# Performance work log

Measured on AMD Instinct MI355X. Metric: run time of the kernel, lower is better.

## Reference

```python
import jax, jax.numpy as jnp
import numpy as np

K = 64        # num_clusters
S1 = 5        # num_shadow + 1
C = 128       # dim
ALPHA = 1500.0
EPS = 1e-12


def setup_inputs() -> dict:
    key = jax.random.key(0)
    k1, k2 = jax.random.split(key)
    x = jax.random.normal(k1, (8, C, 44, 44), dtype=jnp.float32)
    centroids = jax.random.normal(k2, (K, S1, C), dtype=jnp.float32) * 0.01
    return {"x": x, "centroids": centroids}


def reference(x, centroids):
    N = x.shape[0]
    # conv params derived from centroids, as in _init_params
    w = (2.0 * ALPHA) * centroids.reshape(K * S1, C)            # (K*S1, C)
    b = -ALPHA * jnp.linalg.norm(centroids.reshape(K * S1, C), axis=1)  # (K*S1,)

    xf = x.reshape(N, C, -1)                                    # (N, C, P)
    # 1x1 conv == GEMM over channel dim
    logits = jnp.einsum('mc,ncp->nmp', w, xf) + b[None, :, None]
    logits = logits.reshape(N, K, S1, -1)                       # (N, K, S1, P)

    soft_alpha = jax.nn.softmax(logits[:, :, 0:1, :], axis=1)   # (N, K, 1, P)
    soft_beta = jax.nn.softmax(logits, axis=2)[:, :, 0:1, :]    # (N, K, 1, P)
    soft_assign = soft_alpha * soft_beta                        # (N, K, 1, P)

    # residual = x - rep_centroid; then residual *= (1 + soft_assign); sum over P.
    # sum_p (x[n,c,p] - rep[k,c]) * w[n,k,p]
    #   = einsum(w, x) - rep[k,c] * sum_p w[n,k,p]   (same math, no (N,K,C,P) tensor)
    w_assign = 1.0 + soft_assign[:, :, 0, :]                    # (N, K, P)
    rep = centroids[:, 0, :]                                    # (K, C)
    out = jnp.einsum('nkp,ncp->nkc', w_assign, xf) \
          - rep[None, :, :] * jnp.sum(w_assign, axis=-1)[:, :, None]  # (N, K, C)

    # intra-cluster L2 normalize (dim=2), flatten, global L2 normalize
    out = out / jnp.maximum(jnp.linalg.norm(out, axis=2, keepdims=True), EPS)
    flat = out.reshape(N, -1)
    flat = flat / jnp.maximum(jnp.linalg.norm(flat, axis=1, keepdims=True), EPS)
    return (flat, soft_assign)
```

## Files before the change

### kernel.cpp

```cpp
#include <hip/hip_runtime.h>
#include <math.h>

#define NB 8
#define KC 64
#define S1C 5
#define CC 128
#define PP 1936
#define MM 320
#define PT 64
#define NPT 31
#define NTILE (NB * NPT)
#define ALPHAF 1500.0f
#define EPSF 1e-12f

#define WS_CENPK 65536
#define WS_GBIAS 512
#define WS_HDR   (WS_CENPK + WS_GBIAS)
#define WS_PART  ((size_t)NTILE * KC * CC)
#define WS_MAIN_FLOATS (WS_HDR + WS_PART + (size_t)NTILE * KC)

typedef __attribute__((ext_vector_type(8))) short short8;
typedef __attribute__((ext_vector_type(4))) float f32x4;

__device__ __forceinline__ void split8(const float4 a, const float4 b,
                                       short8& h, short8& l) {
    const float f[8] = {a.x, a.y, a.z, a.w, b.x, b.y, b.z, b.w};
#pragma unroll
    for (int j = 0; j < 8; ++j) {
        const unsigned u  = __float_as_uint(f[j]);
        const unsigned hi = u & 0xffff0000u;
        const float lo    = f[j] - __uint_as_float(hi);
        h[j] = (short)(hi >> 16);
        l[j] = (short)(__float_as_uint(lo) >> 16);
    }
}

__global__ __launch_bounds__(64) void k0_pack(
    const float* __restrict__ cen, unsigned* __restrict__ cenPk,
    float* __restrict__ gbias)
{
    const int nt   = blockIdx.x;
    const int l    = threadIdx.x;
    const int l15  = l & 15;
    const int quad = l >> 4;
    const int mp   = nt * 16 + l15;
    const int s    = mp & 7;
    const bool valid = (s < 5);
    const int wrow = 5 * (mp >> 3) + s;
    short8* dst8 = (short8*)cenPk;
    float ss = 0.f;
#pragma unroll
    for (int ks = 0; ks < 4; ++ks) {
        float4 v0 = make_float4(0.f, 0.f, 0.f, 0.f), v1 = v0;
        if (valid) {
            const float* wp = cen + (size_t)wrow * CC + ks * 32 + quad * 8;
            v0 = *(const float4*)wp;
            v1 = *(const float4*)(wp + 4);
        }
        ss += v0.x * v0.x + v0.y * v0.y + v0.z * v0.z + v0.w * v0.w
            + v1.x * v1.x + v1.y * v1.y + v1.z * v1.z + v1.w * v1.w;
        short8 h, lo;
        split8(v0, v1, h, lo);
        const int base = ((ks * 32 + nt) * 64 + l) * 2;
        dst8[base]     = h;
        dst8[base + 1] = lo;
    }
    ss += __shfl_xor(ss, 16);
    ss += __shfl_xor(ss, 32);
    if (quad == 0) gbias[mp] = valid ? (-ALPHAF * sqrtf(ss)) : -3.0e38f;
}

__global__ __launch_bounds__(1024, 4) void k1_main(
    const float* __restrict__ x, const unsigned* __restrict__ cenPk,
    const float* __restrict__ gbias,
    float* __restrict__ sa_out, float* __restrict__ outC,
    float* __restrict__ outS, int mode)
{
    __shared__ __align__(16) unsigned short xh [64 * 128];
    __shared__ __align__(16) unsigned short xl [64 * 128];
    __shared__ __align__(16) unsigned short xch[128 * 64];
    __shared__ __align__(16) unsigned short xcl[128 * 64];
    __shared__ __align__(16) unsigned short wah[64 * 64];
    __shared__ __align__(16) unsigned short wal[64 * 64];
    __shared__ float2 ap[16 * 66];

    const int tid  = threadIdx.x;
    const int lane = tid & 63;
    const int wid  = tid >> 6;
    const int quad = lane >> 4;
    const int l15  = lane & 15;
    const int bx   = blockIdx.x;
    const int n    = bx / NPT;
    const int pt   = bx - n * NPT;
    const int p0   = pt * PT;

    float4 bvf[2];
#pragma unroll
    for (int i = 0; i < 2; ++i)
        bvf[i] = *(const float4*)(gbias + (2 * wid + i) * 16 + quad * 4);
    const short8* cpk8 = (const short8*)cenPk;
    short8 ch0[2], cl0[2];
#pragma unroll
    for (int i = 0; i < 2; ++i) {
        const int boff = ((2 * wid + i) * 64 + lane) * 2;
        ch0[i] = cpk8[boff];
        cl0[i] = cpk8[boff + 1];
    }

    const float* xn = x + (size_t)n * CC * PP;
    {
        const int pl = tid & 63;
        const int c0 = (tid >> 6) * 8;
        const bool pv = (p0 + pl) < PP;
        const float* src = xn + p0 + pl;
        float v[8];
#pragma unroll
        for (int i = 0; i < 8; ++i)
            v[i] = pv ? src[(size_t)(c0 + i) * PP] : 0.f;
        unsigned short hv[8], lv[8];
#pragma unroll
        for (int i = 0; i < 8; ++i) {
            const unsigned u  = __float_as_uint(v[i]);
            const unsigned hi = u & 0xffff0000u;
            hv[i] = (unsigned short)(hi >> 16);
            lv[i] = (unsigned short)(__float_as_uint(v[i] - __uint_as_float(hi)) >> 16);
        }
        short8 H8, L8;
#pragma unroll
        for (int i = 0; i < 8; ++i) { H8[i] = (short)hv[i]; L8[i] = (short)lv[i]; }
        const int sx = (pl * 128 + c0) ^ ((pl & 7) << 3);
        *(short8*)&xh[sx] = H8;
        *(short8*)&xl[sx] = L8;
#pragma unroll
        for (int i = 0; i < 8; ++i) {
            const int ci  = c0 + i;
            const int sc2 = (ci * 64 + pl) ^ ((ci & 7) << 3);
            xch[sc2] = hv[i];
            xcl[sc2] = lv[i];
        }
    }
    __syncthreads();

    f32x4 dacc[4][2];
#pragma unroll
    for (int a = 0; a < 4; ++a) {
        dacc[a][0] = (f32x4){0.f, 0.f, 0.f, 0.f};
        dacc[a][1] = (f32x4){0.f, 0.f, 0.f, 0.f};
    }

    auto mfma_step = [&](const int ksoff, const short8 ch[2], const short8 cl[2]) {
#pragma unroll
        for (int a = 0; a < 4; ++a) {
            const int arow = a * 16 + l15;
            const int sidx = (arow * 128 + ksoff + quad * 8) ^ ((arow & 7) << 3);
            const short8 xh8 = *(const short8*)&xh[sidx];
            const short8 xl8 = *(const short8*)&xl[sidx];
#pragma unroll
            for (int i = 0; i < 2; ++i) {
                dacc[a][i] = __builtin_amdgcn_mfma_f32_16x16x32_bf16(ch[i], xh8, dacc[a][i], 0, 0, 0);
                dacc[a][i] = __builtin_amdgcn_mfma_f32_16x16x32_bf16(ch[i], xl8, dacc[a][i], 0, 0, 0);
                dacc[a][i] = __builtin_amdgcn_mfma_f32_16x16x32_bf16(cl[i], xh8, dacc[a][i], 0, 0, 0);
            }
        }
    };

    mfma_step(0, ch0, cl0);
#pragma unroll 1
    for (int ks = 1; ks < 4; ++ks) {
        short8 ch[2], cl[2];
#pragma unroll
        for (int i = 0; i < 2; ++i) {
            const int boff = ((ks * 32 + 2 * wid + i) * 64 + lane) * 2;
            ch[i] = cpk8[boff];
            cl[i] = cpk8[boff + 1];
        }
        mfma_step(ks * 32, ch, cl);
    }

#pragma unroll
    for (int i = 0; i < 2; ++i) {
        const float* bvp = (const float*)&bvf[i];
#pragma unroll
        for (int a = 0; a < 4; ++a)
#pragma unroll
            for (int r = 0; r < 4; ++r)
                dacc[a][i][r] = 2.f * ALPHAF * dacc[a][i][r] + bvp[r];
    }

#pragma unroll
    for (int a = 0; a < 4; ++a) {
        const float l0 = dacc[a][0][0];
        const float l1 = dacc[a][1][0];
        const float m2 = fmaxf(l0, l1);
        const float mo = __shfl_xor(m2, 32);
        const float m4 = fmaxf(m2, mo);
        float se = __expf(l0 - m4) + __expf(l1 - m4);
        se += __shfl_xor(se, 32);
        if ((lane & 48) == 0) ap[wid * 66 + a * 16 + l15] = make_float2(m4, se);
    }
    __syncthreads();

    float gmv, arv;
    {
        float gm = -3.0e38f;
#pragma unroll
        for (int w = 0; w < 16; ++w) gm = fmaxf(gm, ap[w * 66 + lane].x);
        float s = 0.f;
#pragma unroll
        for (int w = 0; w < 16; ++w) {
            const float2 v = ap[w * 66 + lane];
            s += v.y * __expf(v.x - gm);
        }
        gmv = gm; arv = 1.0f / s;
    }

    const int  kb  = 4 * wid + ((lane >> 5) & 1);
    const bool evq = ((lane & 16) == 0);
    float psum2[2] = {0.f, 0.f};
#pragma unroll
    for (int a = 0; a < 4; ++a) {
        const int p = a * 16 + l15;
        const float gm_p = __shfl(gmv, p);
        const float ar_p = __shfl(arv, p);
        const bool pvalid = (p0 + p) < PP;
#pragma unroll
        for (int i = 0; i < 2; ++i) {
            const f32x4 lg = dacc[a][i];
            const float s4 = __shfl_xor(lg[0], 16);
            float m5 = fmaxf(fmaxf(lg[0], lg[1]), fmaxf(lg[2], lg[3]));
            m5 = fmaxf(m5, s4);
            const float e0 = __expf(lg[0] - m5);
            const float d5 = e0 + __expf(lg[1] - m5) + __expf(lg[2] - m5)
                           + __expf(lg[3] - m5) + __expf(s4 - m5);
            const float sa = __expf(lg[0] - gm_p) * ar_p * (e0 / d5);
            const float wa = pvalid ? (1.0f + sa) : 0.0f;
            if (evq) {
                const int kk = kb + 2 * i;
                const int si = (kk * 64 + p) ^ ((kk & 7) << 3);
                const unsigned u  = __float_as_uint(wa);
                const unsigned hi = u & 0xffff0000u;
                wah[si] = (unsigned short)(hi >> 16);
                wal[si] = (unsigned short)(__float_as_uint(wa - __uint_as_float(hi)) >> 16);
            }
            psum2[i] += wa;
        }
    }
#pragma unroll
    for (int i = 0; i < 2; ++i) {
        float s = psum2[i];
        s += __shfl_xor(s, 1);
        s += __shfl_xor(s, 2);
        s += __shfl_xor(s, 4);
        s += __shfl_xor(s, 8);
        if ((lane & 31) == 0) {
            const int k = kb + 2 * i;
            if (mode == 0) outS[(size_t)bx * KC + k] = s;
            else           atomicAdd(&outS[(size_t)n * KC + k], s);
        }
    }
    __syncthreads();

    const int kt  = wid & 3;
    const int ct0 = (wid >> 2) * 2;
    f32x4 cacc[2];
    cacc[0] = (f32x4){0.f, 0.f, 0.f, 0.f};
    cacc[1] = (f32x4){0.f, 0.f, 0.f, 0.f};
#pragma unroll
    for (int ks = 0; ks < 64; ks += 32) {
        const int arow = kt * 16 + l15;
        const int sa_  = (arow * 64 + ks + quad * 8) ^ ((arow & 7) << 3);
        const short8 ah = *(const short8*)&wah[sa_];
        const short8 al = *(const short8*)&wal[sa_];
#pragma unroll
        for (int t = 0; t < 2; ++t) {
            const int crow = (ct0 + t) * 16 + l15;
            const int sb   = (crow * 64 + ks + quad * 8) ^ ((crow & 7) << 3);
            const short8 bh = *(const short8*)&xch[sb];
            const short8 bl = *(const short8*)&xcl[sb];
            cacc[t] = __builtin_amdgcn_mfma_f32_16x16x32_bf16(ah, bh, cacc[t], 0, 0, 0);
            cacc[t] = __builtin_amdgcn_mfma_f32_16x16x32_bf16(ah, bl, cacc[t], 0, 0, 0);
            cacc[t] = __builtin_amdgcn_mfma_f32_16x16x32_bf16(al, bh, cacc[t], 0, 0, 0);
        }
    }
    if (mode == 0) {
        float* dst = outC + (size_t)bx * KC * CC;
#pragma unroll
        for (int t = 0; t < 2; ++t) {
            const int c = (ct0 + t) * 16 + l15;
#pragma unroll
            for (int r = 0; r < 4; ++r)
                dst[(kt * 16 + 4 * quad + r) * CC + c] = cacc[t][r];
        }
    } else {
        float* dst = outC + (size_t)n * KC * CC;
#pragma unroll
        for (int t = 0; t < 2; ++t) {
            const int c = (ct0 + t) * 16 + l15;
#pragma unroll
            for (int r = 0; r < 4; ++r)
                atomicAdd(&dst[(kt * 16 + 4 * quad + r) * CC + c], cacc[t][r]);
        }
    }

    {
        float* san = sa_out + (size_t)n * KC * PP;
        const int k  = tid >> 4;
        const int p4 = (tid & 15) * 4;
        const int pg = p0 + p4;
        if (pg < PP) {
            const int si = (k * 64 + p4) ^ ((k & 7) << 3);
            const uint2 qh = *(const uint2*)&wah[si];
            const uint2 ql = *(const uint2*)&wal[si];
            const unsigned hh[2] = {qh.x, qh.y};
            const unsigned ll[2] = {ql.x, ql.y};
            float4 sv; float* svp = &sv.x;
#pragma unroll
            for (int j = 0; j < 4; ++j) {
                const unsigned h16 = (hh[j >> 1] >> ((j & 1) * 16)) & 0xffffu;
                const unsigned l16 = (ll[j >> 1] >> ((j & 1) * 16)) & 0xffffu;
                const float wa = __uint_as_float(h16 << 16) + __uint_as_float(l16 << 16);
                svp[j] = wa - 1.0f;
            }
            *(float4*)&san[(size_t)k * PP + pg] = sv;
        }
    }
}

__global__ __launch_bounds__(128) void k2_slab(
    const float* __restrict__ part, const float* __restrict__ ps,
    const float* __restrict__ cen, float* __restrict__ flat)
{
    __shared__ float w2[2];
    const int b = blockIdx.x;
    const int n = b >> 6;
    const int k = b & 63;
    const int c = threadIdx.x;
    const float* pb = part + (size_t)n * NPT * KC * CC + (size_t)k * CC + c;
    float v = 0.f;
#pragma unroll 8
    for (int pt = 0; pt < NPT; ++pt) v += pb[(size_t)pt * KC * CC];
    const float* psb = ps + (size_t)n * NPT * KC + k;
    float sw = 0.f;
#pragma unroll
    for (int pt = 0; pt < NPT; ++pt) sw += psb[(size_t)pt * KC];
    v -= cen[(size_t)k * S1C * CC + c] * sw;

    float ss = v * v;
#pragma unroll
    for (int off = 32; off > 0; off >>= 1) ss += __shfl_down(ss, off);
    if ((c & 63) == 0) w2[c >> 6] = ss;
    __syncthreads();
    const float norm = sqrtf(w2[0] + w2[1]);
    const float scale = 1.0f / (fmaxf(norm, EPSF) * 8.0f);
    flat[(size_t)b * CC + c] = v * scale;
}

__global__ __launch_bounds__(128) void k2_final(
    const float* __restrict__ accC, const float* __restrict__ accS,
    const float* __restrict__ cen, float* __restrict__ flat)
{
    __shared__ float w2[2];
    const int b = blockIdx.x;
    const int k = b & 63;
    const int c = threadIdx.x;
    const float v = accC[(size_t)b * CC + c] -
                    cen[(size_t)k * S1C * CC + c] * accS[b];
    float ss = v * v;
#pragma unroll
    for (int off = 32; off > 0; off >>= 1) ss += __shfl_down(ss, off);
    if ((c & 63) == 0) w2[c >> 6] = ss;
    __syncthreads();
    const float norm = sqrtf(w2[0] + w2[1]);
    const float scale = 1.0f / (fmaxf(norm, EPSF) * 8.0f);
    flat[(size_t)b * CC + c] = v * scale;
}

extern "C" void kernel_launch(void* const* d_in, const int* in_sizes, int n_in,
                              void* d_out, int out_size, void* d_ws, size_t ws_size,
                              hipStream_t stream) {
    const float* x   = (const float*)d_in[0];
    const float* cen = (const float*)d_in[1];
    float* out  = (float*)d_out;
    float* flat = out;
    float* sa   = out + (size_t)NB * KC * CC;
    float* ws   = (float*)d_ws;

    unsigned* cenPk = (unsigned*)ws;
    float*    gbias = ws + WS_CENPK;

    if (ws_size >= WS_MAIN_FLOATS * 4) {
        float* part = ws + WS_HDR;
        float* ps   = part + WS_PART;
        k0_pack<<<32, 64, 0, stream>>>(cen, cenPk, gbias);
        k1_main<<<NTILE, 1024, 0, stream>>>(x, cenPk, gbias, sa, part, ps, 0);
        k2_slab<<<NB * KC, 128, 0, stream>>>(part, ps, cen, flat);
    } else {
        float* accC = ws + WS_HDR;
        float* accS = accC + (size_t)NB * KC * CC;
        hipMemsetAsync(accC, 0, (size_t)(NB * KC * CC + NB * KC) * 4, stream);
        k0_pack<<<32, 64, 0, stream>>>(cen, cenPk, gbias);
        k1_main<<<NTILE, 1024, 0, stream>>>(x, cenPk, gbias, sa, accC, accS, 1);
        k2_final<<<NB * KC, 128, 0, stream>>>(accC, accS, cen, flat);
    }
}
```

Measured before the change: 81.56 us.

## Fuse pack, main, and slab kernels into one persistent kernel with grid barriers

```diff
diff --git a/kernel.cpp b/kernel.cpp
--- a/kernel.cpp
+++ b/kernel.cpp
@@ -6,7 +6,6 @@
 #define S1C 5
 #define CC 128
 #define PP 1936
-#define MM 320
 #define PT 64
 #define NPT 31
 #define NTILE (NB * NPT)
@@ -17,7 +16,9 @@
 #define WS_GBIAS 512
 #define WS_HDR   (WS_CENPK + WS_GBIAS)
 #define WS_PART  ((size_t)NTILE * KC * CC)
-#define WS_MAIN_FLOATS (WS_HDR + WS_PART + (size_t)NTILE * KC)
+#define WS_BAR   (WS_HDR + WS_PART + (size_t)NTILE * KC)
+#define WS_TOTAL (WS_BAR + 4)
+#define BAR_MAGIC 0x9E3779B97F4A7C15ull
 
 typedef __attribute__((ext_vector_type(8))) short short8;
 typedef __attribute__((ext_vector_type(4))) float f32x4;
@@ -35,12 +36,27 @@
     }
 }
 
-__global__ __launch_bounds__(64) void k0_pack(
+__device__ __forceinline__ void gbar(unsigned* cnt, unsigned* gen, unsigned nblk) {
+    __syncthreads();
+    if (threadIdx.x == 0) {
+        __threadfence();
+        const unsigned g = __hip_atomic_load(gen, __ATOMIC_ACQUIRE, __HIP_MEMORY_SCOPE_AGENT);
+        const unsigned old = __hip_atomic_fetch_add(cnt, 1u, __ATOMIC_ACQ_REL, __HIP_MEMORY_SCOPE_AGENT);
+        if (old == nblk - 1u) {
+            __hip_atomic_store(cnt, 0u, __ATOMIC_RELAXED, __HIP_MEMORY_SCOPE_AGENT);
+            __hip_atomic_fetch_add(gen, 1u, __ATOMIC_RELEASE, __HIP_MEMORY_SCOPE_AGENT);
+        } else {
+            while (__hip_atomic_load(gen, __ATOMIC_ACQUIRE, __HIP_MEMORY_SCOPE_AGENT) == g)
+                __builtin_amdgcn_s_sleep(8);
+        }
+    }
+    __syncthreads();
+}
+
+__device__ __forceinline__ void k0_body(
     const float* __restrict__ cen, unsigned* __restrict__ cenPk,
-    float* __restrict__ gbias)
+    float* __restrict__ gbias, const int nt, const int l)
 {
-    const int nt   = blockIdx.x;
-    const int l    = threadIdx.x;
     const int l15  = l & 15;
     const int quad = l >> 4;
     const int mp   = nt * 16 + l15;
@@ -70,11 +86,17 @@
     if (quad == 0) gbias[mp] = valid ? (-ALPHAF * sqrtf(ss)) : -3.0e38f;
 }
 
-__global__ __launch_bounds__(1024, 4) void k1_main(
-    const float* __restrict__ x, const unsigned* __restrict__ cenPk,
-    const float* __restrict__ gbias,
-    float* __restrict__ sa_out, float* __restrict__ outC,
-    float* __restrict__ outS, int mode)
+__global__ __launch_bounds__(64) void k0_pack(
+    const float* __restrict__ cen, unsigned* __restrict__ cenPk,
+    float* __restrict__ gbias)
+{
+    k0_body(cen, cenPk, gbias, blockIdx.x, threadIdx.x);
+}
+
+__global__ __launch_bounds__(1024, 4) void k_fused(
+    const float* __restrict__ x, const float* __restrict__ cen,
+    float* __restrict__ ws, float* __restrict__ sa_out,
+    float* __restrict__ flat)
 {
     __shared__ __align__(16) unsigned short xh [64 * 128];
     __shared__ __align__(16) unsigned short xl [64 * 128];
@@ -83,6 +105,15 @@
     __shared__ __align__(16) unsigned short wah[64 * 64];
     __shared__ __align__(16) unsigned short wal[64 * 64];
     __shared__ float2 ap[16 * 66];
+    __shared__ float  shw[16];
+
+    unsigned*  cenPk = (unsigned*)ws;
+    float*     gbias = ws + WS_CENPK;
+    float*     part  = ws + WS_HDR;
+    float*     ps    = part + WS_PART;
+    unsigned*  bcnt  = (unsigned*)(ws + WS_BAR);
+    unsigned*  bgen  = bcnt + 1;
+    unsigned long long* bready = (unsigned long long*)(bcnt + 2);
 
     const int tid  = threadIdx.x;
     const int lane = tid & 63;
@@ -94,18 +125,7 @@
     const int pt   = bx - n * NPT;
     const int p0   = pt * PT;
 
-    float4 bvf[2];
-#pragma unroll
-    for (int i = 0; i < 2; ++i)
-        bvf[i] = *(const float4*)(gbias + (2 * wid + i) * 16 + quad * 4);
-    const short8* cpk8 = (const short8*)cenPk;
-    short8 ch0[2], cl0[2];
-#pragma unroll
-    for (int i = 0; i < 2; ++i) {
-        const int boff = ((2 * wid + i) * 64 + lane) * 2;
-        ch0[i] = cpk8[boff];
-        cl0[i] = cpk8[boff + 1];
-    }
+    if (bx < 32 && tid < 64) k0_body(cen, cenPk, gbias, bx, tid);
 
     const float* xn = x + (size_t)n * CC * PP;
     {
@@ -139,7 +159,34 @@
             xcl[sc2] = lv[i];
         }
     }
-    __syncthreads();
+
+    if (tid == 0) {
+        if (bx == 0) {
+            if (__hip_atomic_load(bready, __ATOMIC_ACQUIRE, __HIP_MEMORY_SCOPE_AGENT) != BAR_MAGIC) {
+                __hip_atomic_store(bcnt, 0u, __ATOMIC_RELAXED, __HIP_MEMORY_SCOPE_AGENT);
+                __hip_atomic_store(bgen, 0u, __ATOMIC_RELAXED, __HIP_MEMORY_SCOPE_AGENT);
+                __hip_atomic_store(bready, (unsigned long long)BAR_MAGIC,
+                                   __ATOMIC_RELEASE, __HIP_MEMORY_SCOPE_AGENT);
+            }
+        } else {
+            while (__hip_atomic_load(bready, __ATOMIC_ACQUIRE, __HIP_MEMORY_SCOPE_AGENT) != BAR_MAGIC)
+                __builtin_amdgcn_s_sleep(8);
+        }
+    }
+    gbar(bcnt, bgen, NTILE);
+
+    float4 bvf[2];
+#pragma unroll
+    for (int i = 0; i < 2; ++i)
+        bvf[i] = *(const float4*)(gbias + (2 * wid + i) * 16 + quad * 4);
+    const short8* cpk8 = (const short8*)cenPk;
+    short8 ch0[2], cl0[2];
+#pragma unroll
+    for (int i = 0; i < 2; ++i) {
+        const int boff = ((2 * wid + i) * 64 + lane) * 2;
+        ch0[i] = cpk8[boff];
+        cl0[i] = cpk8[boff + 1];
+    }
 
     f32x4 dacc[4][2];
 #pragma unroll
@@ -252,11 +299,8 @@
         s += __shfl_xor(s, 2);
         s += __shfl_xor(s, 4);
         s += __shfl_xor(s, 8);
-        if ((lane & 31) == 0) {
-            const int k = kb + 2 * i;
-            if (mode == 0) outS[(size_t)bx * KC + k] = s;
-            else           atomicAdd(&outS[(size_t)n * KC + k], s);
-        }
+        if ((lane & 31) == 0)
+            ps[(size_t)bx * KC + kb + 2 * i] = s;
     }
     __syncthreads();
 
@@ -282,23 +326,14 @@
             cacc[t] = __builtin_amdgcn_mfma_f32_16x16x32_bf16(al, bh, cacc[t], 0, 0, 0);
         }
     }
-    if (mode == 0) {
-        float* dst = outC + (size_t)bx * KC * CC;
+    {
+        float* dst = part + (size_t)bx * KC * CC;
 #pragma unroll
         for (int t = 0; t < 2; ++t) {
             const int c = (ct0 + t) * 16 + l15;
 #pragma unroll
             for (int r = 0; r < 4; ++r)
                 dst[(kt * 16 + 4 * quad + r) * CC + c] = cacc[t][r];
-        }
-    } else {
-        float* dst = outC + (size_t)n * KC * CC;
-#pragma unroll
-        for (int t = 0; t < 2; ++t) {
-            const int c = (ct0 + t) * 16 + l15;
-#pragma unroll
-            for (int r = 0; r < 4; ++r)
-                atomicAdd(&dst[(kt * 16 + 4 * quad + r) * CC + c], cacc[t][r]);
         }
     }
 
@@ -324,35 +359,271 @@
             *(float4*)&san[(size_t)k * PP + pg] = sv;
         }
     }
-}
-
-__global__ __launch_bounds__(128) void k2_slab(
-    const float* __restrict__ part, const float* __restrict__ ps,
-    const float* __restrict__ cen, float* __restrict__ flat)
+
+    gbar(bcnt, bgen, NTILE);
+
+    if (bx < 64) {
+        const int slab = bx * 8 + (tid >> 7);
+        const int sn = slab >> 6;
+        const int sk = slab & 63;
+        const int c  = tid & 127;
+        const float* pb = part + (size_t)sn * NPT * KC * CC + (size_t)sk * CC + c;
+        float v = 0.f;
+#pragma unroll 8
+        for (int q = 0; q < NPT; ++q) v += pb[(size_t)q * KC * CC];
+        const float* psb = ps + (size_t)sn * NPT * KC + sk;
+        float sw = 0.f;
+#pragma unroll
+        for (int q = 0; q < NPT; ++q) sw += psb[(size_t)q * KC];
+        v -= cen[(size_t)sk * S1C * CC + c] * sw;
+
+        float ss = v * v;
+#pragma unroll
+        for (int off = 32; off > 0; off >>= 1) ss += __shfl_down(ss, off);
+        if ((c & 63) == 0) shw[(tid >> 7) * 2 + ((c >> 6) & 1)] = ss;
+        __syncthreads();
+        const float norm = sqrtf(shw[(tid >> 7) * 2] + shw[(tid >> 7) * 2 + 1]);
+        const float scale = 1.0f / (fmaxf(norm, EPSF) * 8.0f);
+        flat[(size_t)slab * CC + c] = v * scale;
+    }
+}
+
+__global__ __launch_bounds__(1024, 4) void k1_atomic(
+    const float* __restrict__ x, const unsigned* __restrict__ cenPk,
+    const float* __restrict__ gbias,
+    float* __restrict__ sa_out, float* __restrict__ outC,
+    float* __restrict__ outS)
 {
-    __shared__ float w2[2];
-    const int b = blockIdx.x;
-    const int n = b >> 6;
-    const int k = b & 63;
-    const int c = threadIdx.x;
-    const float* pb = part + (size_t)n * NPT * KC * CC + (size_t)k * CC + c;
-    float v = 0.f;
-#pragma unroll 8
-    for (int pt = 0; pt < NPT; ++pt) v += pb[(size_t)pt * KC * CC];
-    const float* psb = ps + (size_t)n * NPT * KC + k;
-    float sw = 0.f;
-#pragma unroll
-    for (int pt = 0; pt < NPT; ++pt) sw += psb[(size_t)pt * KC];
-    v -= cen[(size_t)k * S1C * CC + c] * sw;
-
-    float ss = v * v;
-#pragma unroll
-    for (int off = 32; off > 0; off >>= 1) ss += __shfl_down(ss, off);
-    if ((c & 63) == 0) w2[c >> 6] = ss;
-    __syncthreads();
-    const float norm = sqrtf(w2[0] + w2[1]);
-    const float scale = 1.0f / (fmaxf(norm, EPSF) * 8.0f);
-    flat[(size_t)b * CC + c] = v * scale;
+    __shared__ __align__(16) unsigned short xh [64 * 128];
+    __shared__ __align__(16) unsigned short xl [64 * 128];
+    __shared__ __align__(16) unsigned short xch[128 * 64];
+    __shared__ __align__(16) unsigned short xcl[128 * 64];
+    __shared__ __align__(16) unsigned short wah[64 * 64];
+    __shared__ __align__(16) unsigned short wal[64 * 64];
+    __shared__ float2 ap[16 * 66];
+
+    const int tid  = threadIdx.x;
+    const int lane = tid & 63;
+    const int wid  = tid >> 6;
+    const int quad = lane >> 4;
+    const int l15  = lane & 15;
+    const int bx   = blockIdx.x;
+    const int n    = bx / NPT;
+    const int pt   = bx - n * NPT;
+    const int p0   = pt * PT;
+
+    float4 bvf[2];
+#pragma unroll
+    for (int i = 0; i < 2; ++i)
+        bvf[i] = *(const float4*)(gbias + (2 * wid + i) * 16 + quad * 4);
+    const short8* cpk8 = (const short8*)cenPk;
+    short8 ch0[2], cl0[2];
+#pragma unroll
+    for (int i = 0; i < 2; ++i) {
+        const int boff = ((2 * wid + i) * 64 + lane) * 2;
+        ch0[i] = cpk8[boff];
+        cl0[i] = cpk8[boff + 1];
+    }
+
+    const float* xn = x + (size_t)n * CC * PP;
+    {
+        const int pl = tid & 63;
+        const int c0 = (tid >> 6) * 8;
+        const bool pv = (p0 + pl) < PP;
+        const float* src = xn + p0 + pl;
+        float v[8];
+#pragma unroll
+        for (int i = 0; i < 8; ++i)
+            v[i] = pv ? src[(size_t)(c0 + i) * PP] : 0.f;
+        unsigned short hv[8], lv[8];
+#pragma unroll
+        for (int i = 0; i < 8; ++i) {
+            const unsigned u  = __float_as_uint(v[i]);
+            const unsigned hi = u & 0xffff0000u;
+            hv[i] = (unsigned short)(hi >> 16);
+            lv[i] = (unsigned short)(__float_as_uint(v[i] - __uint_as_float(hi)) >> 16);
+        }
+        short8 H8, L8;
+#pragma unroll
+        for (int i = 0; i < 8; ++i) { H8[i] = (short)hv[i]; L8[i] = (short)lv[i]; }
+        const int sx = (pl * 128 + c0) ^ ((pl & 7) << 3);
+        *(short8*)&xh[sx] = H8;
+        *(short8*)&xl[sx] = L8;
+#pragma unroll
+        for (int i = 0; i < 8; ++i) {
+            const int ci  = c0 + i;
+            const int sc2 = (ci * 64 + pl) ^ ((ci & 7) << 3);
+            xch[sc2] = hv[i];
+            xcl[sc2] = lv[i];
+        }
+    }
+    __syncthreads();
+
+    f32x4 dacc[4][2];
+#pragma unroll
+    for (int a = 0; a < 4; ++a) {
+        dacc[a][0] = (f32x4){0.f, 0.f, 0.f, 0.f};
+        dacc[a][1] = (f32x4){0.f, 0.f, 0.f, 0.f};
+    }
+    auto mfma_step = [&](const int ksoff, const short8 ch[2], const short8 cl[2]) {
+#pragma unroll
+        for (int a = 0; a < 4; ++a) {
+            const int arow = a * 16 + l15;
+            const int sidx = (arow * 128 + ksoff + quad * 8) ^ ((arow & 7) << 3);
+            const short8 xh8 = *(const short8*)&xh[sidx];
+            const short8 xl8 = *(const short8*)&xl[sidx];
+#pragma unroll
+            for (int i = 0; i < 2; ++i) {
+                dacc[a][i] = __builtin_amdgcn_mfma_f32_16x16x32_bf16(ch[i], xh8, dacc[a][i], 0, 0, 0);
+                dacc[a][i] = __builtin_amdgcn_mfma_f32_16x16x32_bf16(ch[i], xl8, dacc[a][i], 0, 0, 0);
+                dacc[a][i] = __builtin_amdgcn_mfma_f32_16x16x32_bf16(cl[i], xh8, dacc[a][i], 0, 0, 0);
+            }
+        }
+    };
+    mfma_step(0, ch0, cl0);
+#pragma unroll 1
+    for (int ks = 1; ks < 4; ++ks) {
+        short8 ch[2], cl[2];
+#pragma unroll
+        for (int i = 0; i < 2; ++i) {
+            const int boff = ((ks * 32 + 2 * wid + i) * 64 + lane) * 2;
+            ch[i] = cpk8[boff];
+            cl[i] = cpk8[boff + 1];
+        }
+        mfma_step(ks * 32, ch, cl);
+    }
+#pragma unroll
+    for (int i = 0; i < 2; ++i) {
+        const float* bvp = (const float*)&bvf[i];
+#pragma unroll
+        for (int a = 0; a < 4; ++a)
+#pragma unroll
+            for (int r = 0; r < 4; ++r)
+                dacc[a][i][r] = 2.f * ALPHAF * dacc[a][i][r] + bvp[r];
+    }
+#pragma unroll
+    for (int a = 0; a < 4; ++a) {
+        const float l0 = dacc[a][0][0];
+        const float l1 = dacc[a][1][0];
+        const float m2 = fmaxf(l0, l1);
+        const float mo = __shfl_xor(m2, 32);
+        const float m4 = fmaxf(m2, mo);
+        float se = __expf(l0 - m4) + __expf(l1 - m4);
+        se += __shfl_xor(se, 32);
+        if ((lane & 48) == 0) ap[wid * 66 + a * 16 + l15] = make_float2(m4, se);
+    }
+    __syncthreads();
+
+    float gmv, arv;
+    {
+        float gm = -3.0e38f;
+#pragma unroll
+        for (int w = 0; w < 16; ++w) gm = fmaxf(gm, ap[w * 66 + lane].x);
+        float s = 0.f;
+#pragma unroll
+        for (int w = 0; w < 16; ++w) {
+            const float2 v = ap[w * 66 + lane];
+            s += v.y * __expf(v.x - gm);
+        }
+        gmv = gm; arv = 1.0f / s;
+    }
+    const int  kb  = 4 * wid + ((lane >> 5) & 1);
+    const bool evq = ((lane & 16) == 0);
+    float psum2[2] = {0.f, 0.f};
+#pragma unroll
+    for (int a = 0; a < 4; ++a) {
+        const int p = a * 16 + l15;
+        const float gm_p = __shfl(gmv, p);
+        const float ar_p = __shfl(arv, p);
+        const bool pvalid = (p0 + p) < PP;
+#pragma unroll
+        for (int i = 0; i < 2; ++i) {
+            const f32x4 lg = dacc[a][i];
+            const float s4 = __shfl_xor(lg[0], 16);
+            float m5 = fmaxf(fmaxf(lg[0], lg[1]), fmaxf(lg[2], lg[3]));
+            m5 = fmaxf(m5, s4);
+            const float e0 = __expf(lg[0] - m5);
+            const float d5 = e0 + __expf(lg[1] - m5) + __expf(lg[2] - m5)
+                           + __expf(lg[3] - m5) + __expf(s4 - m5);
+            const float sa = __expf(lg[0] - gm_p) * ar_p * (e0 / d5);
+            const float wa = pvalid ? (1.0f + sa) : 0.0f;
+            if (evq) {
+                const int kk = kb + 2 * i;
+                const int si = (kk * 64 + p) ^ ((kk & 7) << 3);
+                const unsigned u  = __float_as_uint(wa);
+                const unsigned hi = u & 0xffff0000u;
+                wah[si] = (unsigned short)(hi >> 16);
+                wal[si] = (unsigned short)(__float_as_uint(wa - __uint_as_float(hi)) >> 16);
+            }
+            psum2[i] += wa;
+        }
+    }
+#pragma unroll
+    for (int i = 0; i < 2; ++i) {
+        float s = psum2[i];
+        s += __shfl_xor(s, 1);
+        s += __shfl_xor(s, 2);
+        s += __shfl_xor(s, 4);
+        s += __shfl_xor(s, 8);
+        if ((lane & 31) == 0)
+            atomicAdd(&outS[(size_t)n * KC + kb + 2 * i], s);
+    }
+    __syncthreads();
+
+    const int kt  = wid & 3;
+    const int ct0 = (wid >> 2) * 2;
+    f32x4 cacc[2];
+    cacc[0] = (f32x4){0.f, 0.f, 0.f, 0.f};
+    cacc[1] = (f32x4){0.f, 0.f, 0.f, 0.f};
+#pragma unroll
+    for (int ks = 0; ks < 64; ks += 32) {
+        const int arow = kt * 16 + l15;
+        const int sa_  = (arow * 64 + ks + quad * 8) ^ ((arow & 7) << 3);
+        const short8 ah = *(const short8*)&wah[sa_];
+        const short8 al = *(const short8*)&wal[sa_];
+#pragma unroll
+        for (int t = 0; t < 2; ++t) {
+            const int crow = (ct0 + t) * 16 + l15;
+            const int sb   = (crow * 64 + ks + quad * 8) ^ ((crow & 7) << 3);
+            const short8 bh = *(const short8*)&xch[sb];
+            const short8 bl = *(const short8*)&xcl[sb];
+            cacc[t] = __builtin_amdgcn_mfma_f32_16x16x32_bf16(ah, bh, cacc[t], 0, 0, 0);
+            cacc[t] = __builtin_amdgcn_mfma_f32_16x16x32_bf16(ah, bl, cacc[t], 0, 0, 0);
+            cacc[t] = __builtin_amdgcn_mfma_f32_16x16x32_bf16(al, bh, cacc[t], 0, 0, 0);
+        }
+    }
+    {
+        float* dst = outC + (size_t)n * KC * CC;
+#pragma unroll
+        for (int t = 0; t < 2; ++t) {
+            const int c = (ct0 + t) * 16 + l15;
+#pragma unroll
+            for (int r = 0; r < 4; ++r)
+                atomicAdd(&dst[(kt * 16 + 4 * quad + r) * CC + c], cacc[t][r]);
+        }
+    }
+    {
+        float* san = sa_out + (size_t)n * KC * PP;
+        const int k  = tid >> 4;
+        const int p4 = (tid & 15) * 4;
+        const int pg = p0 + p4;
+        if (pg < PP) {
+            const int si = (k * 64 + p4) ^ ((k & 7) << 3);
+            const uint2 qh = *(const uint2*)&wah[si];
+            const uint2 ql = *(const uint2*)&wal[si];
+            const unsigned hh[2] = {qh.x, qh.y};
+            const unsigned ll[2] = {ql.x, ql.y};
+            float4 sv; float* svp = &sv.x;
+#pragma unroll
+            for (int j = 0; j < 4; ++j) {
+                const unsigned h16 = (hh[j >> 1] >> ((j & 1) * 16)) & 0xffffu;
+                const unsigned l16 = (ll[j >> 1] >> ((j & 1) * 16)) & 0xffffu;
+                const float wa = __uint_as_float(h16 << 16) + __uint_as_float(l16 << 16);
+                svp[j] = wa - 1.0f;
+            }
+            *(float4*)&san[(size_t)k * PP + pg] = sv;
+        }
+    }
 }
 
 __global__ __launch_bounds__(128) void k2_final(
@@ -385,21 +656,16 @@
     float* sa   = out + (size_t)NB * KC * CC;
     float* ws   = (float*)d_ws;
 
-    unsigned* cenPk = (unsigned*)ws;
-    float*    gbias = ws + WS_CENPK;
-
-    if (ws_size >= WS_MAIN_FLOATS * 4) {
-        float* part = ws + WS_HDR;
-        float* ps   = part + WS_PART;
-        k0_pack<<<32, 64, 0, stream>>>(cen, cenPk, gbias);
-        k1_main<<<NTILE, 1024, 0, stream>>>(x, cenPk, gbias, sa, part, ps, 0);
-        k2_slab<<<NB * KC, 128, 0, stream>>>(part, ps, cen, flat);
+    if (ws_size >= WS_TOTAL * 4) {
+        k_fused<<<NTILE, 1024, 0, stream>>>(x, cen, ws, sa, flat);
     } else {
-        float* accC = ws + WS_HDR;
-        float* accS = accC + (size_t)NB * KC * CC;
+        unsigned* cenPk = (unsigned*)ws;
+        float*    gbias = ws + WS_CENPK;
+        float*    accC  = ws + WS_HDR;
+        float*    accS  = accC + (size_t)NB * KC * CC;
         hipMemsetAsync(accC, 0, (size_t)(NB * KC * CC + NB * KC) * 4, stream);
         k0_pack<<<32, 64, 0, stream>>>(cen, cenPk, gbias);
-        k1_main<<<NTILE, 1024, 0, stream>>>(x, cenPk, gbias, sa, accC, accS, 1);
+        k1_atomic<<<NTILE, 1024, 0, stream>>>(x, cenPk, gbias, sa, accC, accS);
         k2_final<<<NB * KC, 128, 0, stream>>>(accC, accS, cen, flat);
     }
 }
```

Measured after the change: 149.6 us. +83.4%, slower.
